# Performance work log

Measured on AMD Instinct MI355X. Metric: run time of the kernel, lower is better.

The kernel has to match this reference:

```python
import jax, jax.numpy as jnp
from jax import lax
import numpy as np

B, C, H, W = 16, 64, 256, 256
K = 4


def setup_inputs() -> dict:
    key = jax.random.key(0)
    k1, k2, k3, k4 = jax.random.split(key, 4)
    x = jax.random.normal(k1, (B, C, H, W), dtype=jnp.float32)
    weight = jax.random.normal(k2, (K, C, 3, 3), dtype=jnp.float32)
    # attn 1x1 conv: weight [K, C] (squeezed 1x1 spatial), bias [K]
    attn_w = jax.random.normal(k3, (K, C), dtype=jnp.float32) * (1.0 / np.sqrt(C))
    attn_b = jax.random.normal(k4, (K,), dtype=jnp.float32) * 0.01
    return {"x": x, "weight": weight, "attn_w": attn_w, "attn_b": attn_b}


def reference(x, weight, attn_w, attn_b):
    # 1x1 conv -> logits [B, K, H, W], then softmax over the K kernels
    logits = jnp.einsum("bchw,kc->bkhw", x, attn_w) + attn_b[None, :, None, None]
    attn = jax.nn.softmax(logits, axis=1)
    # One grouped call producing all K single-channel conv outputs: [B, K, H, W]
    conv = lax.conv_general_dilated(
        x, weight,
        window_strides=(1, 1), padding="SAME",
        dimension_numbers=("NCHW", "OIHW", "NCHW"),
    )
    # attention-weighted mixture, summed over kernels -> [B, 1, H, W]
    return jnp.sum(conv * attn, axis=1, keepdims=True)
```

## Files before the change

### kernel.cpp

```cpp
#include <hip/hip_runtime.h>


#define HH 256
#define WW 256
#define CH 64
#define TILE 32
#define CPB 2
#define NG (CH / CPB)
#define ROWS 34
#define NC4 10
#define LDSS 41
#define CH_STRIDE (ROWS * LDSS)
#define TV (CPB * ROWS * NC4)
#define NS 3

__global__ __launch_bounds__(256, 4) void kwdc_fused(
    const float* __restrict__ x,
    const float* __restrict__ weight,
    const float* __restrict__ attn_w,
    const float* __restrict__ attn_b,
    float* __restrict__ out)
{
    __shared__ float lds[2][CPB * CH_STRIDE];

    const int tid = threadIdx.x;

    const int fid = blockIdx.x;
    const int tw = (fid >> 3) & 7;
    const int th = fid & 7;
    const int b  = fid >> 6;

    const int r  = tid >> 3;
    const int cg = tid & 7;
    const int wb = cg * 4;

    const int h0 = th * TILE;
    const int w0 = tw * TILE;

    const float* xb = x + (size_t)b * CH * HH * WW;

    int  s_ch[NS];
    int  s_gofs[NS];
    int  s_lofs[NS];
    bool s_val[NS];
    bool s_act[NS];
#pragma unroll
    for (int s = 0; s < NS; ++s) {
        int i = tid + s * 256;
        bool act = i < TV;
        int col4  = i % NC4;
        int rowch = i / NC4;
        int row   = rowch % ROWS;
        int ch    = rowch / ROWS;
        int gh  = h0 + row - 1;
        int gw0 = w0 - 4 + col4 * 4;
        s_act[s]  = act;
        s_val[s]  = act && ((unsigned)gh < HH) && ((unsigned)gw0 < WW);
        s_gofs[s] = gh * WW + gw0;
        s_lofs[s] = ch * CH_STRIDE + row * LDSS + col4 * 4;
        s_ch[s]   = ch;
    }

    float4 stgA[NS], stgB[NS];

    auto load_set = [&](int g, float4* stg) {
#pragma unroll
        for (int s = 0; s < NS; ++s) {
            float4 v = {0.f, 0.f, 0.f, 0.f};
            if (s_val[s]) {
                const float* p = xb + (size_t)(g * CPB + s_ch[s]) * (HH * WW) + s_gofs[s];
                v = *reinterpret_cast<const float4*>(p);
            }
            stg[s] = v;
        }
    };

    auto store_set = [&](const float4* stg, int buf) {
#pragma unroll
        for (int s = 0; s < NS; ++s) {
            if (s_act[s]) {
                float* q = &lds[buf][s_lofs[s]];
                q[0] = stg[s].x; q[1] = stg[s].y; q[2] = stg[s].z; q[3] = stg[s].w;
            }
        }
    };

    float conv[4][4];
    float logit[4][4];
#pragma unroll
    for (int k = 0; k < 4; ++k)
#pragma unroll
        for (int p = 0; p < 4; ++p) { conv[k][p] = 0.f; logit[k][p] = 0.f; }

    load_set(0, stgA);
    store_set(stgA, 0);
    load_set(1, stgA);
    load_set(2, stgB);
    __syncthreads();

    for (int g = 0; g < NG; ++g) {
        if (g + 1 < NG) {
            float4* setp = (g & 1) ? stgB : stgA;
            store_set(setp, (g + 1) & 1);
            if (g + 3 < NG) load_set(g + 3, setp);
        }

#pragma unroll
        for (int c = 0; c < CPB; ++c) {
            const int gc = g * CPB + c;
            const float* tp = &lds[g & 1][c * CH_STRIDE + r * LDSS + wb + 3];
            float rv[3][6];
#pragma unroll
            for (int i = 0; i < 3; ++i)
#pragma unroll
                for (int j = 0; j < 6; ++j)
                    rv[i][j] = tp[i * LDSS + j];

#pragma unroll
            for (int k = 0; k < 4; ++k) {
                const float* wp = weight + (k * CH + gc) * 9;
                const float w00 = wp[0], w01 = wp[1], w02 = wp[2];
                const float w10 = wp[3], w11 = wp[4], w12 = wp[5];
                const float w20 = wp[6], w21 = wp[7], w22 = wp[8];
                const float aw  = attn_w[k * CH + gc];
#pragma unroll
                for (int p = 0; p < 4; ++p) {
                    float acc = conv[k][p];
                    acc = fmaf(rv[0][p],     w00, acc);
                    acc = fmaf(rv[0][p + 1], w01, acc);
                    acc = fmaf(rv[0][p + 2], w02, acc);
                    acc = fmaf(rv[1][p],     w10, acc);
                    acc = fmaf(rv[1][p + 1], w11, acc);
                    acc = fmaf(rv[1][p + 2], w12, acc);
                    acc = fmaf(rv[2][p],     w20, acc);
                    acc = fmaf(rv[2][p + 1], w21, acc);
                    acc = fmaf(rv[2][p + 2], w22, acc);
                    conv[k][p] = acc;
                    logit[k][p] = fmaf(rv[1][p + 1], aw, logit[k][p]);
                }
            }
        }
        __syncthreads();
    }

    const float b0 = attn_b[0], b1 = attn_b[1], b2 = attn_b[2], b3 = attn_b[3];
    float4 o;
    float* op = &o.x;
#pragma unroll
    for (int p = 0; p < 4; ++p) {
        float l0 = logit[0][p] + b0;
        float l1 = logit[1][p] + b1;
        float l2 = logit[2][p] + b2;
        float l3 = logit[3][p] + b3;
        float m = fmaxf(fmaxf(l0, l1), fmaxf(l2, l3));
        float e0 = __expf(l0 - m), e1 = __expf(l1 - m);
        float e2 = __expf(l2 - m), e3 = __expf(l3 - m);
        float s = e0 + e1 + e2 + e3;
        float num = conv[0][p] * e0 + conv[1][p] * e1
                  + conv[2][p] * e2 + conv[3][p] * e3;
        op[p] = num / s;
    }
    size_t oidx = (size_t)b * HH * WW + (size_t)(h0 + r) * WW + (w0 + wb);
    *reinterpret_cast<float4*>(out + oidx) = o;
}

extern "C" void kernel_launch(void* const* d_in, const int* in_sizes, int n_in,
                              void* d_out, int out_size, void* d_ws, size_t ws_size,
                              hipStream_t stream) {
    const float* x      = (const float*)d_in[0];
    const float* weight = (const float*)d_in[1];
    const float* attn_w = (const float*)d_in[2];
    const float* attn_b = (const float*)d_in[3];
    float* out = (float*)d_out;

    kwdc_fused<<<dim3(1024, 1, 1), 256, 0, stream>>>(x, weight, attn_w, attn_b, out);
}
```

Baseline: 91.38 us.

## Pack channel pairs to fp16 in LDS and use dot2 for conv and logits

Converts each pair of input channels to packed fp16 (round-toward-zero) when staging into LDS. Weights and attention weights are pre-packed the same way by a small separate kernel. The inner loop then uses fdot2 to do two channels per instruction, halving FMA count and LDS footprint and reads. Accumulation stays in fp32, but rounding inputs to fp16 loses precision and could break tolerance. It also adds an extra kernel launch.

Measured after the change: 82.25 us. -10.0%, faster.

```diff
diff --git a/kernel.cpp b/kernel.cpp
--- a/kernel.cpp
+++ b/kernel.cpp
@@ -1,27 +1,64 @@
 #include <hip/hip_runtime.h>
 
+
+typedef _Float16 half2_t __attribute__((ext_vector_type(2)));
+typedef unsigned int uint;
 
 #define HH 256
 #define WW 256
 #define CH 64
+#define PLANE (HH * WW)
 #define TILE 32
-#define CPB 2
-#define NG (CH / CPB)
+#define NG 32
 #define ROWS 34
 #define NC4 10
 #define LDSS 41
-#define CH_STRIDE (ROWS * LDSS)
-#define TV (CPB * ROWS * NC4)
-#define NS 3
-
-__global__ __launch_bounds__(256, 4) void kwdc_fused(
+#define BUF_DW (ROWS * LDSS)
+#define TU (ROWS * NC4)
+#define NS 2
+
+#define WPK_N 1152
+#define APK_OFF 1152
+
+__device__ __forceinline__ uint pkrtz(float a, float b) {
+    return __builtin_bit_cast(uint, __builtin_amdgcn_cvt_pkrtz(a, b));
+}
+
+__device__ __forceinline__ float dot2(uint a, uint b, float c) {
+#if __has_builtin(__builtin_amdgcn_fdot2)
+    return __builtin_amdgcn_fdot2(__builtin_bit_cast(half2_t, a),
+                                  __builtin_bit_cast(half2_t, b), c, false);
+#else
+    half2_t ha = __builtin_bit_cast(half2_t, a);
+    half2_t hb = __builtin_bit_cast(half2_t, b);
+    return c + (float)ha[0] * (float)hb[0] + (float)ha[1] * (float)hb[1];
+#endif
+}
+
+__global__ void kwdc_pack(const float* __restrict__ weight,
+                          const float* __restrict__ attn_w,
+                          uint* __restrict__ wsu) {
+    int e = blockIdx.x * 256 + threadIdx.x;
+    if (e < WPK_N) {
+        int k = e / 288, rem = e % 288, pair = rem / 9, tap = rem % 9;
+        int c0 = 2 * pair;
+        wsu[e] = pkrtz(weight[(k * CH + c0) * 9 + tap],
+                       weight[(k * CH + c0 + 1) * 9 + tap]);
+    } else if (e < WPK_N + 128) {
+        int e2 = e - WPK_N;
+        int k = e2 / 32, pair = e2 % 32;
+        int c0 = 2 * pair;
+        wsu[APK_OFF + e2] = pkrtz(attn_w[k * CH + c0], attn_w[k * CH + c0 + 1]);
+    }
+}
+
+__global__ __launch_bounds__(256, 4) void kwdc_main(
     const float* __restrict__ x,
-    const float* __restrict__ weight,
-    const float* __restrict__ attn_w,
+    const uint*  __restrict__ wsu,
     const float* __restrict__ attn_b,
     float* __restrict__ out)
 {
-    __shared__ float lds[2][CPB * CH_STRIDE];
+    __shared__ uint lds[2][BUF_DW];
 
     const int tid = threadIdx.x;
 
@@ -37,9 +74,8 @@
     const int h0 = th * TILE;
     const int w0 = tw * TILE;
 
-    const float* xb = x + (size_t)b * CH * HH * WW;
-
-    int  s_ch[NS];
+    const float* xb = x + (size_t)b * CH * PLANE;
+
     int  s_gofs[NS];
     int  s_lofs[NS];
     bool s_val[NS];
@@ -47,40 +83,42 @@
 #pragma unroll
     for (int s = 0; s < NS; ++s) {
         int i = tid + s * 256;
-        bool act = i < TV;
-        int col4  = i % NC4;
-        int rowch = i / NC4;
-        int row   = rowch % ROWS;
-        int ch    = rowch / ROWS;
+        bool act = i < TU;
+        int col4 = i % NC4;
+        int row  = i / NC4;
         int gh  = h0 + row - 1;
         int gw0 = w0 - 4 + col4 * 4;
         s_act[s]  = act;
         s_val[s]  = act && ((unsigned)gh < HH) && ((unsigned)gw0 < WW);
         s_gofs[s] = gh * WW + gw0;
-        s_lofs[s] = ch * CH_STRIDE + row * LDSS + col4 * 4;
-        s_ch[s]   = ch;
-    }
-
-    float4 stgA[NS], stgB[NS];
-
-    auto load_set = [&](int g, float4* stg) {
+        s_lofs[s] = row * LDSS + col4 * 4;
+    }
+
+    struct Unit { float4 a, b; };
+    Unit stgA[NS], stgB[NS];
+
+    auto load_set = [&](int g, Unit* stg) {
 #pragma unroll
         for (int s = 0; s < NS; ++s) {
-            float4 v = {0.f, 0.f, 0.f, 0.f};
+            float4 va = {0.f, 0.f, 0.f, 0.f}, vb = va;
             if (s_val[s]) {
-                const float* p = xb + (size_t)(g * CPB + s_ch[s]) * (HH * WW) + s_gofs[s];
-                v = *reinterpret_cast<const float4*>(p);
+                const float* pa = xb + (size_t)(2 * g) * PLANE + s_gofs[s];
+                va = *reinterpret_cast<const float4*>(pa);
+                vb = *reinterpret_cast<const float4*>(pa + PLANE);
             }
-            stg[s] = v;
+            stg[s].a = va; stg[s].b = vb;
         }
     };
 
-    auto store_set = [&](const float4* stg, int buf) {
+    auto store_set = [&](const Unit* stg, int buf) {
 #pragma unroll
         for (int s = 0; s < NS; ++s) {
             if (s_act[s]) {
-                float* q = &lds[buf][s_lofs[s]];
-                q[0] = stg[s].x; q[1] = stg[s].y; q[2] = stg[s].z; q[3] = stg[s].w;
+                uint* q = &lds[buf][s_lofs[s]];
+                q[0] = pkrtz(stg[s].a.x, stg[s].b.x);
+                q[1] = pkrtz(stg[s].a.y, stg[s].b.y);
+                q[2] = pkrtz(stg[s].a.z, stg[s].b.z);
+                q[3] = pkrtz(stg[s].a.w, stg[s].b.w);
             }
         }
     };
@@ -100,44 +138,45 @@
 
     for (int g = 0; g < NG; ++g) {
         if (g + 1 < NG) {
-            float4* setp = (g & 1) ? stgB : stgA;
+            Unit* setp = (g & 1) ? stgB : stgA;
             store_set(setp, (g + 1) & 1);
             if (g + 3 < NG) load_set(g + 3, setp);
         }
 
-#pragma unroll
-        for (int c = 0; c < CPB; ++c) {
-            const int gc = g * CPB + c;
-            const float* tp = &lds[g & 1][c * CH_STRIDE + r * LDSS + wb + 3];
-            float rv[3][6];
-#pragma unroll
-            for (int i = 0; i < 3; ++i)
-#pragma unroll
-                for (int j = 0; j < 6; ++j)
-                    rv[i][j] = tp[i * LDSS + j];
-
-#pragma unroll
-            for (int k = 0; k < 4; ++k) {
-                const float* wp = weight + (k * CH + gc) * 9;
-                const float w00 = wp[0], w01 = wp[1], w02 = wp[2];
-                const float w10 = wp[3], w11 = wp[4], w12 = wp[5];
-                const float w20 = wp[6], w21 = wp[7], w22 = wp[8];
-                const float aw  = attn_w[k * CH + gc];
-#pragma unroll
-                for (int p = 0; p < 4; ++p) {
-                    float acc = conv[k][p];
-                    acc = fmaf(rv[0][p],     w00, acc);
-                    acc = fmaf(rv[0][p + 1], w01, acc);
-                    acc = fmaf(rv[0][p + 2], w02, acc);
-                    acc = fmaf(rv[1][p],     w10, acc);
-                    acc = fmaf(rv[1][p + 1], w11, acc);
-                    acc = fmaf(rv[1][p + 2], w12, acc);
-                    acc = fmaf(rv[2][p],     w20, acc);
-                    acc = fmaf(rv[2][p + 1], w21, acc);
-                    acc = fmaf(rv[2][p + 2], w22, acc);
-                    conv[k][p] = acc;
-                    logit[k][p] = fmaf(rv[1][p + 1], aw, logit[k][p]);
-                }
+        uint w2[4][9];
+        uint a2[4];
+#pragma unroll
+        for (int k = 0; k < 4; ++k) {
+            const uint* wq = wsu + k * 288 + g * 9;
+#pragma unroll
+            for (int t = 0; t < 9; ++t) w2[k][t] = wq[t];
+            a2[k] = wsu[APK_OFF + k * 32 + g];
+        }
+
+        const uint* tp = &lds[g & 1][r * LDSS + wb + 3];
+        uint rv[3][6];
+#pragma unroll
+        for (int i = 0; i < 3; ++i)
+#pragma unroll
+            for (int j = 0; j < 6; ++j)
+                rv[i][j] = tp[i * LDSS + j];
+
+#pragma unroll
+        for (int k = 0; k < 4; ++k) {
+#pragma unroll
+            for (int p = 0; p < 4; ++p) {
+                float acc = conv[k][p];
+                acc = dot2(rv[0][p],     w2[k][0], acc);
+                acc = dot2(rv[0][p + 1], w2[k][1], acc);
+                acc = dot2(rv[0][p + 2], w2[k][2], acc);
+                acc = dot2(rv[1][p],     w2[k][3], acc);
+                acc = dot2(rv[1][p + 1], w2[k][4], acc);
+                acc = dot2(rv[1][p + 2], w2[k][5], acc);
+                acc = dot2(rv[2][p],     w2[k][6], acc);
+                acc = dot2(rv[2][p + 1], w2[k][7], acc);
+                acc = dot2(rv[2][p + 2], w2[k][8], acc);
+                conv[k][p] = acc;
+                logit[k][p] = dot2(rv[1][p + 1], a2[k], logit[k][p]);
             }
         }
         __syncthreads();
@@ -160,7 +199,7 @@
                   + conv[2][p] * e2 + conv[3][p] * e3;
         op[p] = num / s;
     }
-    size_t oidx = (size_t)b * HH * WW + (size_t)(h0 + r) * WW + (w0 + wb);
+    size_t oidx = (size_t)b * PLANE + (size_t)(h0 + r) * WW + (w0 + wb);
     *reinterpret_cast<float4*>(out + oidx) = o;
 }
 
@@ -172,6 +211,8 @@
     const float* attn_w = (const float*)d_in[2];
     const float* attn_b = (const float*)d_in[3];
     float* out = (float*)d_out;
-
-    kwdc_fused<<<dim3(1024, 1, 1), 256, 0, stream>>>(x, weight, attn_w, attn_b, out);
-}
+    uint*  wsu = (uint*)d_ws;
+
+    kwdc_pack<<<dim3(5), 256, 0, stream>>>(weight, attn_w, wsu);
+    kwdc_main<<<dim3(1024), 256, 0, stream>>>(x, wsu, attn_b, out);
+}
```
